# Optimization experiments

Hardware: AMD Instinct MI355X
Metric: run time of the kernel (lower is better)

Reference implementation:

```python
import jax, jax.numpy as jnp
import numpy as np

B, N, E, H, D, FF = 4, 4096, 128, 8, 16, 512
EPS = 1e-6


def rmsnorm(x, w):
    return x * jax.lax.rsqrt(jnp.mean(x * x, axis=-1, keepdims=True) + EPS) * w


def setup_inputs() -> dict:
    key = jax.random.key(0)
    ks = jax.random.split(key, 12)
    s = 1.0 / np.sqrt(E)
    return {
        "x": jax.random.normal(ks[0], (B, N, E), jnp.float32),
        "dis_matrix": jax.random.uniform(ks[1], (B, N, N), jnp.float32),
        "g_in": jnp.ones((E,), jnp.float32),
        "g_post": jnp.ones((E,), jnp.float32),
        "Wq": jax.random.normal(ks[2], (E, E), jnp.float32) * s,
        "Wk": jax.random.normal(ks[3], (E, E), jnp.float32) * s,
        "Wv": jax.random.normal(ks[4], (E, E), jnp.float32) * s,
        "alpha": jnp.float32(1.0),
        "Wo": jax.random.normal(ks[5], (H * D, E), jnp.float32) * s,
        "W1": jax.random.normal(ks[6], (E, FF), jnp.float32) * s,
        "b1": jnp.zeros((FF,), jnp.float32),
        "W2": jax.random.normal(ks[7], (FF, E), jnp.float32) / np.sqrt(FF),
        "b2": jnp.zeros((E,), jnp.float32),
    }


def reference(x, dis_matrix, g_in, g_post, Wq, Wk, Wv, alpha, Wo, W1, b1, W2, b2):
    b, n, e = x.shape
    h = rmsnorm(x, g_in)
    # project and split heads: [B,N,E] -> [B,H,N,D]
    def heads(y):
        return y.reshape(b, n, H, D).transpose(0, 2, 1, 3)
    q = heads(h @ Wq)
    k = heads(h @ Wk)
    v = heads(h @ Wv)
    # distance-decayed kernel weights [B,N,N]
    dis_w = jnp.exp(-alpha * np.log2(n) * dis_matrix)
    kw = jnp.exp(k)  # [B,H,N,D]
    w1 = jnp.einsum('bij,bhik->bhjk', dis_w, kw * v)
    w2 = jnp.einsum('bij,bhik->bhjk', dis_w, kw)
    att = jax.nn.sigmoid(q) * (w1 / w2)  # [B,H,N,D]
    att = att.transpose(0, 2, 1, 3).reshape(b, n, e)
    out1 = x + att @ Wo
    h2 = rmsnorm(out1, g_post)
    ff = jax.nn.relu(h2 @ W1 + b1) @ W2 + b2
    return out1 + ff
```

## Files before the change

kernel.cpp:

```cpp
#include <hip/hip_runtime.h>
#include <stdint.h>


typedef __attribute__((ext_vector_type(8))) short short8;
typedef __attribute__((ext_vector_type(4))) float f32x4;

__device__ __forceinline__ uint16_t f2bf(float f) {
    uint32_t u = __builtin_bit_cast(uint32_t, f);
    u += 0x7fffu + ((u >> 16) & 1u);
    return (uint16_t)(u >> 16);
}
__device__ __forceinline__ float bf2f(uint16_t h) {
    uint32_t u = ((uint32_t)h) << 16;
    return __builtin_bit_cast(float, u);
}
__device__ __forceinline__ f32x4 mfma16(short8 a, short8 b, f32x4 c) {
    return __builtin_amdgcn_mfma_f32_16x16x32_bf16(a, b, c, 0, 0, 0);
}

__global__ __launch_bounds__(256) void k_prep(
    const float* __restrict__ Wq, const float* __restrict__ Wk,
    const float* __restrict__ Wv, const float* __restrict__ Wo,
    const float* __restrict__ W1, const float* __restrict__ W2,
    uint16_t* __restrict__ wqkvT, uint16_t* __restrict__ woT,
    uint16_t* __restrict__ w1T, uint16_t* __restrict__ w2T) {
    int t = blockIdx.x * 256 + threadIdx.x;
    if (t < 49152) {
        int n = t >> 7, k = t & 127;
        const float* W = (n < 128) ? Wq : (n < 256) ? Wk : Wv;
        wqkvT[t] = f2bf(W[k * 128 + (n & 127)]);
    } else if (t < 65536) {
        int i = t - 49152; int e = i >> 7, d = i & 127;
        woT[i] = f2bf(Wo[d * 128 + e]);
    } else if (t < 131072) {
        int i = t - 65536; int f = i >> 7, e = i & 127;
        w1T[i] = f2bf(W1[e * 512 + f]);
    } else if (t < 196608) {
        int i = t - 131072; int e = i >> 9, f = i & 511;
        w2T[i] = f2bf(W2[f * 128 + e]);
    }
}

__global__ __launch_bounds__(256) void k_rms(
    const float* __restrict__ x, const float* __restrict__ g,
    uint16_t* __restrict__ o) {
    int row = blockIdx.x * 4 + (threadIdx.x >> 6);
    int l = threadIdx.x & 63;
    float2 v = *(const float2*)(x + (size_t)row * 128 + l * 2);
    float ss = v.x * v.x + v.y * v.y;
    #pragma unroll
    for (int m = 32; m >= 1; m >>= 1) ss += __shfl_xor(ss, m, 64);
    float rs = rsqrtf(ss * (1.0f / 128.0f) + 1e-6f);
    float2 gv = *(const float2*)(g + l * 2);
    uint32_t lo = (uint32_t)f2bf(v.x * rs * gv.x) |
                  ((uint32_t)f2bf(v.y * rs * gv.y) << 16);
    *(uint32_t*)(o + (size_t)row * 128 + l * 2) = lo;
}

__global__ __launch_bounds__(384) void k_qkv(
    const uint16_t* __restrict__ h, const uint16_t* __restrict__ wqkvT,
    uint16_t* __restrict__ sigq, uint16_t* __restrict__ mcatT) {
    __shared__ __align__(16) char sm[65536];
    uint16_t* Al = (uint16_t*)sm;
    float*    Pl = (float*)sm;
    const int t = threadIdx.x;
    const int i0 = blockIdx.x * 64;
    for (int idx = t; idx < 1024; idx += 384) {
        int row = idx >> 4, c8 = (idx & 15) * 8;
        *(uint4*)&Al[row * 136 + c8] =
            *(const uint4*)(h + (size_t)(i0 + row) * 128 + c8);
    }
    __syncthreads();
    const int w = t >> 6, l = t & 63, ml = l & 15, qd = l >> 4;
    f32x4 acc[4][4];
    f32x4 zv = {0.f, 0.f, 0.f, 0.f};
    #pragma unroll
    for (int a = 0; a < 4; ++a)
        #pragma unroll
        for (int b = 0; b < 4; ++b) acc[a][b] = zv;
    #pragma unroll
    for (int kc = 0; kc < 4; ++kc) {
        short8 af[4], bfr[4];
        #pragma unroll
        for (int fm = 0; fm < 4; ++fm)
            af[fm] = *(const short8*)&Al[(fm * 16 + ml) * 136 + kc * 32 + qd * 8];
        #pragma unroll
        for (int fn = 0; fn < 4; ++fn)
            bfr[fn] = *(const short8*)(wqkvT + (w * 64 + fn * 16 + ml) * 128 + kc * 32 + qd * 8);
        #pragma unroll
        for (int fm = 0; fm < 4; ++fm)
            #pragma unroll
            for (int fn = 0; fn < 4; ++fn)
                acc[fm][fn] = mfma16(af[fm], bfr[fn], acc[fm][fn]);
    }
    __syncthreads();
    const int bb = i0 >> 12, il0 = i0 & 4095;
    if (w < 2) {
        #pragma unroll
        for (int fm = 0; fm < 4; ++fm)
            #pragma unroll
            for (int fn = 0; fn < 4; ++fn)
                #pragma unroll
                for (int r = 0; r < 4; ++r) {
                    int row = fm * 16 + qd * 4 + r;
                    int col = w * 64 + fn * 16 + ml;
                    sigq[(size_t)(i0 + row) * 128 + col] =
                        f2bf(1.f / (1.f + __expf(-acc[fm][fn][r])));
                }
    } else {
        int half = (w < 4) ? 0 : 1;
        int cbase = (w - (half ? 4 : 2)) * 64;
        #pragma unroll
        for (int fm = 0; fm < 4; ++fm)
            #pragma unroll
            for (int fn = 0; fn < 4; ++fn)
                #pragma unroll
                for (int r = 0; r < 4; ++r) {
                    int row = fm * 16 + qd * 4 + r;
                    int col = cbase + fn * 16 + ml;
                    float vv = acc[fm][fn][r];
                    if (!half) vv = __expf(vv);
                    Pl[row * 256 + half * 128 + ((col + row) & 127)] = vv;
                }
    }
    __syncthreads();
    for (int idx = t; idx < 16384; idx += 384) {
        int cc = idx >> 6, il = idx & 63;
        int pc = ((cc & 127) + il) & 127;
        float ekw = Pl[il * 256 + pc];
        float val = (cc < 128) ? ekw * Pl[il * 256 + 128 + pc] : ekw;
        mcatT[((size_t)bb * 256 + cc) * 4096 + il0 + il] = f2bf(val);
    }
}

__global__ __launch_bounds__(512) void k_big(
    const float* __restrict__ dis, const uint16_t* __restrict__ mcatT,
    const float* __restrict__ alpha_p, float* __restrict__ wbuf) {
    __shared__ __align__(16) uint16_t Al[128 * 72];
    __shared__ __align__(16) uint16_t Bl[256 * 72];
    const int t = threadIdx.x;
    const int j0 = blockIdx.x * 128;
    const int b  = blockIdx.y;
    const int sp = blockIdx.z;
    const float c = -12.0f * alpha_p[0];
    const int w = t >> 6, l = t & 63, ml = l & 15, qd = l >> 4;
    const int wm = w >> 2, wn = w & 3;
    const int sj4 = (t & 31) * 4, si0 = (t >> 5) * 4;
    const float* disb = dis + (size_t)b * 4096 * 4096;
    const uint16_t* mb = mcatT + (size_t)b * 256 * 4096;

    f32x4 acc[4][4];
    f32x4 zv = {0.f, 0.f, 0.f, 0.f};
    #pragma unroll
    for (int a = 0; a < 4; ++a)
        #pragma unroll
        for (int q = 0; q < 4; ++q) acc[a][q] = zv;

    for (int ks = 0; ks < 32; ++ks) {
        const int ig = sp * 2048 + ks * 64;
        float dv[4][4];
        #pragma unroll
        for (int r = 0; r < 4; ++r) {
            float4 v = *(const float4*)(disb + (size_t)(ig + si0 + r) * 4096 + j0 + sj4);
            dv[r][0] = v.x; dv[r][1] = v.y; dv[r][2] = v.z; dv[r][3] = v.w;
        }
        __syncthreads();
        #pragma unroll
        for (int jj = 0; jj < 4; ++jj) {
            uint32_t lo = (uint32_t)f2bf(__expf(c * dv[0][jj])) |
                          ((uint32_t)f2bf(__expf(c * dv[1][jj])) << 16);
            uint32_t hi = (uint32_t)f2bf(__expf(c * dv[2][jj])) |
                          ((uint32_t)f2bf(__expf(c * dv[3][jj])) << 16);
            uint2 pk = {lo, hi};
            *(uint2*)&Al[(sj4 + jj) * 72 + si0] = pk;
        }
        #pragma unroll
        for (int ii = 0; ii < 4; ++ii) {
            int idx = t + ii * 512;
            int row = idx >> 3, c8 = (idx & 7) * 8;
            *(uint4*)&Bl[row * 72 + c8] =
                *(const uint4*)(mb + (size_t)row * 4096 + ig + c8);
        }
        __syncthreads();
        #pragma unroll
        for (int kc = 0; kc < 2; ++kc) {
            short8 af[4], bfr[4];
            #pragma unroll
            for (int fm = 0; fm < 4; ++fm)
                af[fm] = *(const short8*)&Al[(wm * 64 + fm * 16 + ml) * 72 + kc * 32 + qd * 8];
            #pragma unroll
            for (int fn = 0; fn < 4; ++fn)
                bfr[fn] = *(const short8*)&Bl[(wn * 64 + fn * 16 + ml) * 72 + kc * 32 + qd * 8];
            #pragma unroll
            for (int fm = 0; fm < 4; ++fm)
                #pragma unroll
                for (int fn = 0; fn < 4; ++fn)
                    acc[fm][fn] = mfma16(af[fm], bfr[fn], acc[fm][fn]);
        }
    }
    float* ob = wbuf + ((size_t)(sp * 4 + b) * 4096 + j0) * 256;
    #pragma unroll
    for (int fm = 0; fm < 4; ++fm)
        #pragma unroll
        for (int fn = 0; fn < 4; ++fn) {
            int col = wn * 64 + fn * 16 + ml;
            #pragma unroll
            for (int r = 0; r < 4; ++r) {
                int rowl = wm * 64 + fm * 16 + qd * 4 + r;
                ob[(size_t)rowl * 256 + col] = acc[fm][fn][r];
            }
        }
}

__global__ __launch_bounds__(256) void k_att(
    const float* __restrict__ wbuf, const uint16_t* __restrict__ sigq,
    const uint16_t* __restrict__ woT, const float* __restrict__ x,
    float* __restrict__ out1) {
    __shared__ __align__(16) uint16_t Al[64 * 136];
    __shared__ __align__(16) uint16_t Bl[128 * 136];
    const int t = threadIdx.x;
    const int i0 = blockIdx.x * 64;
    const int b = i0 >> 12, jl0 = i0 & 4095;
    const float* wb0 = wbuf + ((size_t)b * 4096 + jl0) * 256;
    const float* wb1 = wbuf + ((size_t)(4 + b) * 4096 + jl0) * 256;
    #pragma unroll
    for (int ii = 0; ii < 8; ++ii) {
        int idx = t + ii * 256;
        int row = idx >> 5, c4 = (idx & 31) * 4;
        float4 a0 = *(const float4*)(wb0 + (size_t)row * 256 + c4);
        float4 a1 = *(const float4*)(wb1 + (size_t)row * 256 + c4);
        float4 d0 = *(const float4*)(wb0 + (size_t)row * 256 + 128 + c4);
        float4 d1 = *(const float4*)(wb1 + (size_t)row * 256 + 128 + c4);
        const uint16_t* sq = sigq + (size_t)(i0 + row) * 128 + c4;
        uint32_t lo = (uint32_t)f2bf(bf2f(sq[0]) * (a0.x + a1.x) / (d0.x + d1.x)) |
                      ((uint32_t)f2bf(bf2f(sq[1]) * (a0.y + a1.y) / (d0.y + d1.y)) << 16);
        uint32_t hi = (uint32_t)f2bf(bf2f(sq[2]) * (a0.z + a1.z) / (d0.z + d1.z)) |
                      ((uint32_t)f2bf(bf2f(sq[3]) * (a0.w + a1.w) / (d0.w + d1.w)) << 16);
        uint2 pk = {lo, hi};
        *(uint2*)&Al[row * 136 + c4] = pk;
    }
    #pragma unroll
    for (int ii = 0; ii < 8; ++ii) {
        int idx = t + ii * 256;
        int row = idx >> 4, c8 = (idx & 15) * 8;
        *(uint4*)&Bl[row * 136 + c8] = *(const uint4*)(woT + row * 128 + c8);
    }
    __syncthreads();
    const int w = t >> 6, l = t & 63, ml = l & 15, qd = l >> 4;
    const int wm = w >> 1, wn = w & 1;
    f32x4 acc[2][4];
    f32x4 zv = {0.f, 0.f, 0.f, 0.f};
    #pragma unroll
    for (int a = 0; a < 2; ++a)
        #pragma unroll
        for (int q = 0; q < 4; ++q) acc[a][q] = zv;
    #pragma unroll
    for (int kc = 0; kc < 4; ++kc) {
        short8 af[2], bfr[4];
        #pragma unroll
        for (int fm = 0; fm < 2; ++fm)
            af[fm] = *(const short8*)&Al[(wm * 32 + fm * 16 + ml) * 136 + kc * 32 + qd * 8];
        #pragma unroll
        for (int fn = 0; fn < 4; ++fn)
            bfr[fn] = *(const short8*)&Bl[(wn * 64 + fn * 16 + ml) * 136 + kc * 32 + qd * 8];
        #pragma unroll
        for (int fm = 0; fm < 2; ++fm)
            #pragma unroll
            for (int fn = 0; fn < 4; ++fn)
                acc[fm][fn] = mfma16(af[fm], bfr[fn], acc[fm][fn]);
    }
    #pragma unroll
    for (int fm = 0; fm < 2; ++fm)
        #pragma unroll
        for (int fn = 0; fn < 4; ++fn) {
            int col = wn * 64 + fn * 16 + ml;
            #pragma unroll
            for (int r = 0; r < 4; ++r) {
                int rowl = wm * 32 + fm * 16 + qd * 4 + r;
                size_t o = (size_t)(i0 + rowl) * 128 + col;
                out1[o] = x[o] + acc[fm][fn][r];
            }
        }
}

__global__ __launch_bounds__(256) void k_ff1(
    const uint16_t* __restrict__ h2, const uint16_t* __restrict__ w1T,
    const float* __restrict__ b1, uint16_t* __restrict__ R) {
    __shared__ __align__(16) uint16_t Al[64 * 136];
    __shared__ __align__(16) uint16_t Bl[128 * 136];
    const int t = threadIdx.x;
    const int i0 = blockIdx.x * 64;
    const int nt = blockIdx.y;
    #pragma unroll
    for (int ii = 0; ii < 4; ++ii) {
        int idx = t + ii * 256;
        int row = idx >> 4, c8 = (idx & 15) * 8;
        *(uint4*)&Al[row * 136 + c8] =
            *(const uint4*)(h2 + (size_t)(i0 + row) * 128 + c8);
    }
    #pragma unroll
    for (int ii = 0; ii < 8; ++ii) {
        int idx = t + ii * 256;
        int row = idx >> 4, c8 = (idx & 15) * 8;
        *(uint4*)&Bl[row * 136 + c8] =
            *(const uint4*)(w1T + (size_t)(nt * 128 + row) * 128 + c8);
    }
    __syncthreads();
    const int w = t >> 6, l = t & 63, ml = l & 15, qd = l >> 4;
    const int wm = w >> 1, wn = w & 1;
    f32x4 acc[2][4];
    f32x4 zv = {0.f, 0.f, 0.f, 0.f};
    #pragma unroll
    for (int a = 0; a < 2; ++a)
        #pragma unroll
        for (int q = 0; q < 4; ++q) acc[a][q] = zv;
    #pragma unroll
    for (int kc = 0; kc < 4; ++kc) {
        short8 af[2], bfr[4];
        #pragma unroll
        for (int fm = 0; fm < 2; ++fm)
            af[fm] = *(const short8*)&Al[(wm * 32 + fm * 16 + ml) * 136 + kc * 32 + qd * 8];
        #pragma unroll
        for (int fn = 0; fn < 4; ++fn)
            bfr[fn] = *(const short8*)&Bl[(wn * 64 + fn * 16 + ml) * 136 + kc * 32 + qd * 8];
        #pragma unroll
        for (int fm = 0; fm < 2; ++fm)
            #pragma unroll
            for (int fn = 0; fn < 4; ++fn)
                acc[fm][fn] = mfma16(af[fm], bfr[fn], acc[fm][fn]);
    }
    #pragma unroll
    for (int fm = 0; fm < 2; ++fm)
        #pragma unroll
        for (int fn = 0; fn < 4; ++fn) {
            int col = wn * 64 + fn * 16 + ml;
            int gcol = nt * 128 + col;
            #pragma unroll
            for (int r = 0; r < 4; ++r) {
                int rowl = wm * 32 + fm * 16 + qd * 4 + r;
                R[(size_t)(i0 + rowl) * 512 + gcol] =
                    f2bf(fmaxf(acc[fm][fn][r] + b1[gcol], 0.f));
            }
        }
}

__global__ __launch_bounds__(256) void k_ff2(
    const uint16_t* __restrict__ Rm, const uint16_t* __restrict__ w2T,
    const float* __restrict__ b2, const float* __restrict__ out1,
    float* __restrict__ out) {
    __shared__ __align__(16) uint16_t Al[64 * 136];
    __shared__ __align__(16) uint16_t Bl[128 * 136];
    const int t = threadIdx.x;
    const int i0 = blockIdx.x * 64;
    const int w = t >> 6, l = t & 63, ml = l & 15, qd = l >> 4;
    const int wm = w >> 1, wn = w & 1;
    f32x4 acc[2][4];
    f32x4 zv = {0.f, 0.f, 0.f, 0.f};
    #pragma unroll
    for (int a = 0; a < 2; ++a)
        #pragma unroll
        for (int q = 0; q < 4; ++q) acc[a][q] = zv;
    for (int kb = 0; kb < 4; ++kb) {
        __syncthreads();
        #pragma unroll
        for (int ii = 0; ii < 4; ++ii) {
            int idx = t + ii * 256;
            int row = idx >> 4, c8 = (idx & 15) * 8;
            *(uint4*)&Al[row * 136 + c8] =
                *(const uint4*)(Rm + (size_t)(i0 + row) * 512 + kb * 128 + c8);
        }
        #pragma unroll
        for (int ii = 0; ii < 8; ++ii) {
            int idx = t + ii * 256;
            int row = idx >> 4, c8 = (idx & 15) * 8;
            *(uint4*)&Bl[row * 136 + c8] =
                *(const uint4*)(w2T + (size_t)row * 512 + kb * 128 + c8);
        }
        __syncthreads();
        #pragma unroll
        for (int kc = 0; kc < 4; ++kc) {
            short8 af[2], bfr[4];
            #pragma unroll
            for (int fm = 0; fm < 2; ++fm)
                af[fm] = *(const short8*)&Al[(wm * 32 + fm * 16 + ml) * 136 + kc * 32 + qd * 8];
            #pragma unroll
            for (int fn = 0; fn < 4; ++fn)
                bfr[fn] = *(const short8*)&Bl[(wn * 64 + fn * 16 + ml) * 136 + kc * 32 + qd * 8];
            #pragma unroll
            for (int fm = 0; fm < 2; ++fm)
                #pragma unroll
                for (int fn = 0; fn < 4; ++fn)
                    acc[fm][fn] = mfma16(af[fm], bfr[fn], acc[fm][fn]);
        }
    }
    #pragma unroll
    for (int fm = 0; fm < 2; ++fm)
        #pragma unroll
        for (int fn = 0; fn < 4; ++fn) {
            int col = wn * 64 + fn * 16 + ml;
            #pragma unroll
            for (int r = 0; r < 4; ++r) {
                int rowl = wm * 32 + fm * 16 + qd * 4 + r;
                size_t o = (size_t)(i0 + rowl) * 128 + col;
                out[o] = out1[o] + b2[col] + acc[fm][fn][r];
            }
        }
}

extern "C" void kernel_launch(void* const* d_in, const int* in_sizes, int n_in,
                              void* d_out, int out_size, void* d_ws, size_t ws_size,
                              hipStream_t stream) {
    (void)in_sizes; (void)n_in; (void)out_size; (void)ws_size;
    const float* x      = (const float*)d_in[0];
    const float* dis    = (const float*)d_in[1];
    const float* g_in   = (const float*)d_in[2];
    const float* g_post = (const float*)d_in[3];
    const float* Wq     = (const float*)d_in[4];
    const float* Wk     = (const float*)d_in[5];
    const float* Wv     = (const float*)d_in[6];
    const float* alpha  = (const float*)d_in[7];
    const float* Wo     = (const float*)d_in[8];
    const float* W1     = (const float*)d_in[9];
    const float* b1     = (const float*)d_in[10];
    const float* W2     = (const float*)d_in[11];
    const float* b2     = (const float*)d_in[12];
    float* out = (float*)d_out;

    char* ws = (char*)d_ws;
    size_t off = 0;
    auto take = [&](size_t bytes) -> char* {
        char* p = ws + off;
        off += (bytes + 255) & ~(size_t)255;
        return p;
    };
    uint16_t* h     = (uint16_t*)take(16384ull * 128 * 2);
    uint16_t* wqkvT = (uint16_t*)take(384ull * 128 * 2);
    uint16_t* woT   = (uint16_t*)take(128ull * 128 * 2);
    uint16_t* w1T   = (uint16_t*)take(512ull * 128 * 2);
    uint16_t* w2T   = (uint16_t*)take(128ull * 512 * 2);
    uint16_t* sigq  = (uint16_t*)take(16384ull * 128 * 2);
    uint16_t* mcatT = (uint16_t*)take(4ull * 256 * 4096 * 2);
    float*    wbuf  = (float*)take(2ull * 4 * 4096 * 256 * 4);
    float*    out1  = (float*)take(16384ull * 128 * 4);
    uint16_t* h2    = (uint16_t*)take(16384ull * 128 * 2);
    uint16_t* R     = (uint16_t*)take(16384ull * 512 * 2);

    k_prep<<<768, 256, 0, stream>>>(Wq, Wk, Wv, Wo, W1, W2, wqkvT, woT, w1T, w2T);
    k_rms<<<4096, 256, 0, stream>>>(x, g_in, h);
    k_qkv<<<256, 384, 0, stream>>>(h, wqkvT, sigq, mcatT);
    k_big<<<dim3(32, 4, 2), 512, 0, stream>>>(dis, mcatT, alpha, wbuf);
    k_att<<<256, 256, 0, stream>>>(wbuf, sigq, woT, x, out1);
    k_rms<<<4096, 256, 0, stream>>>(out1, g_post, h2);
    k_ff1<<<dim3(256, 4), 256, 0, stream>>>(h2, w1T, b1, R);
    k_ff2<<<256, 256, 0, stream>>>(R, w2T, b2, out1, out);
}
```

Measured before the change: 467.1 us.

## Fuse distance-kernel GEMM with attention epilogue, Wo, RMSNorm; fuse FF layers

Replaces the split-K big GEMM plus separate attention, RMSNorm and two FF kernels with one kernel that computes the full K range per 32-column tile. That kernel register-prefetches the next dis/mcat tile, then applies the sigmoid-q ratio, the Wo projection, the residual and the post-RMSNorm in-block. A second kernel fuses FF1, ReLU and FF2, keeping the hidden activations in shared memory, so the wbuf and R intermediates and three launches go away. The risk is that the smaller 32-wide tiles give less MFMA reuse per block and only a quarter of the threads do the exp conversion, and the grid drops from 256 large blocks to 512 smaller ones with no split-K.

After: 699.3 us. 49.7% more time.

```diff
diff --git a/kernel.cpp b/kernel.cpp
--- a/kernel.cpp
+++ b/kernel.cpp
@@ -133,276 +133,255 @@
     }
 }
 
-__global__ __launch_bounds__(512) void k_big(
+__global__ __launch_bounds__(512, 4) void k_mega(
     const float* __restrict__ dis, const uint16_t* __restrict__ mcatT,
-    const float* __restrict__ alpha_p, float* __restrict__ wbuf) {
-    __shared__ __align__(16) uint16_t Al[128 * 72];
-    __shared__ __align__(16) uint16_t Bl[256 * 72];
+    const float* __restrict__ alpha_p, const uint16_t* __restrict__ sigq,
+    const uint16_t* __restrict__ woT, const float* __restrict__ x,
+    const float* __restrict__ g_post,
+    float* __restrict__ out1, uint16_t* __restrict__ h2) {
+    __shared__ __align__(16) char sm[42496];
+    uint16_t* Al = (uint16_t*)sm;
+    uint16_t* Bl = (uint16_t*)(sm + 4608);
+    float*    P  = (float*)sm;
+    uint16_t* Att= (uint16_t*)(sm + 33792);
+    __shared__ float rowsum[32];
+
     const int t = threadIdx.x;
-    const int j0 = blockIdx.x * 128;
+    const int j0 = blockIdx.x * 32;
     const int b  = blockIdx.y;
-    const int sp = blockIdx.z;
     const float c = -12.0f * alpha_p[0];
     const int w = t >> 6, l = t & 63, ml = l & 15, qd = l >> 4;
-    const int wm = w >> 2, wn = w & 3;
-    const int sj4 = (t & 31) * 4, si0 = (t >> 5) * 4;
-    const float* disb = dis + (size_t)b * 4096 * 4096;
+    const bool aload = (t < 128);
+    const int sj4 = (t & 7) * 4, si0 = ((t >> 3) & 15) * 4;
+    const float* disb = dis + (size_t)b * 4096 * 4096 + j0;
     const uint16_t* mb = mcatT + (size_t)b * 256 * 4096;
 
-    f32x4 acc[4][4];
+    f32x4 acc[2][2];
     f32x4 zv = {0.f, 0.f, 0.f, 0.f};
-    #pragma unroll
-    for (int a = 0; a < 4; ++a)
-        #pragma unroll
-        for (int q = 0; q < 4; ++q) acc[a][q] = zv;
-
-    for (int ks = 0; ks < 32; ++ks) {
-        const int ig = sp * 2048 + ks * 64;
-        float dv[4][4];
+    acc[0][0] = zv; acc[0][1] = zv; acc[1][0] = zv; acc[1][1] = zv;
+
+    float dv[4][4];
+    uint4 mc[4];
+    if (aload) {
         #pragma unroll
         for (int r = 0; r < 4; ++r) {
-            float4 v = *(const float4*)(disb + (size_t)(ig + si0 + r) * 4096 + j0 + sj4);
+            float4 v = *(const float4*)(disb + (size_t)(si0 + r) * 4096 + sj4);
             dv[r][0] = v.x; dv[r][1] = v.y; dv[r][2] = v.z; dv[r][3] = v.w;
         }
+    }
+    #pragma unroll
+    for (int ii = 0; ii < 4; ++ii) {
+        int idx = t + ii * 512;
+        int row = idx >> 3, c8 = (idx & 7) * 8;
+        mc[ii] = *(const uint4*)(mb + (size_t)row * 4096 + c8);
+    }
+
+    for (int ks = 0; ks < 64; ++ks) {
         __syncthreads();
-        #pragma unroll
-        for (int jj = 0; jj < 4; ++jj) {
-            uint32_t lo = (uint32_t)f2bf(__expf(c * dv[0][jj])) |
-                          ((uint32_t)f2bf(__expf(c * dv[1][jj])) << 16);
-            uint32_t hi = (uint32_t)f2bf(__expf(c * dv[2][jj])) |
-                          ((uint32_t)f2bf(__expf(c * dv[3][jj])) << 16);
-            uint2 pk = {lo, hi};
-            *(uint2*)&Al[(sj4 + jj) * 72 + si0] = pk;
+        if (aload) {
+            #pragma unroll
+            for (int jj = 0; jj < 4; ++jj) {
+                uint32_t lo = (uint32_t)f2bf(__expf(c * dv[0][jj])) |
+                              ((uint32_t)f2bf(__expf(c * dv[1][jj])) << 16);
+                uint32_t hi = (uint32_t)f2bf(__expf(c * dv[2][jj])) |
+                              ((uint32_t)f2bf(__expf(c * dv[3][jj])) << 16);
+                uint2 pk = {lo, hi};
+                *(uint2*)&Al[(sj4 + jj) * 72 + si0] = pk;
+            }
         }
         #pragma unroll
         for (int ii = 0; ii < 4; ++ii) {
             int idx = t + ii * 512;
             int row = idx >> 3, c8 = (idx & 7) * 8;
-            *(uint4*)&Bl[row * 72 + c8] =
-                *(const uint4*)(mb + (size_t)row * 4096 + ig + c8);
+            *(uint4*)&Bl[row * 72 + c8] = mc[ii];
         }
         __syncthreads();
+        if (ks < 63) {
+            const int ig = (ks + 1) * 64;
+            if (aload) {
+                #pragma unroll
+                for (int r = 0; r < 4; ++r) {
+                    float4 v = *(const float4*)(disb + (size_t)(ig + si0 + r) * 4096 + sj4);
+                    dv[r][0] = v.x; dv[r][1] = v.y; dv[r][2] = v.z; dv[r][3] = v.w;
+                }
+            }
+            #pragma unroll
+            for (int ii = 0; ii < 4; ++ii) {
+                int idx = t + ii * 512;
+                int row = idx >> 3, c8 = (idx & 7) * 8;
+                mc[ii] = *(const uint4*)(mb + (size_t)row * 4096 + ig + c8);
+            }
+        }
         #pragma unroll
         for (int kc = 0; kc < 2; ++kc) {
-            short8 af[4], bfr[4];
-            #pragma unroll
-            for (int fm = 0; fm < 4; ++fm)
-                af[fm] = *(const short8*)&Al[(wm * 64 + fm * 16 + ml) * 72 + kc * 32 + qd * 8];
-            #pragma unroll
-            for (int fn = 0; fn < 4; ++fn)
-                bfr[fn] = *(const short8*)&Bl[(wn * 64 + fn * 16 + ml) * 72 + kc * 32 + qd * 8];
-            #pragma unroll
-            for (int fm = 0; fm < 4; ++fm)
-                #pragma unroll
-                for (int fn = 0; fn < 4; ++fn)
-                    acc[fm][fn] = mfma16(af[fm], bfr[fn], acc[fm][fn]);
-        }
-    }
-    float* ob = wbuf + ((size_t)(sp * 4 + b) * 4096 + j0) * 256;
-    #pragma unroll
-    for (int fm = 0; fm < 4; ++fm)
-        #pragma unroll
-        for (int fn = 0; fn < 4; ++fn) {
-            int col = wn * 64 + fn * 16 + ml;
-            #pragma unroll
-            for (int r = 0; r < 4; ++r) {
-                int rowl = wm * 64 + fm * 16 + qd * 4 + r;
-                ob[(size_t)rowl * 256 + col] = acc[fm][fn][r];
-            }
-        }
-}
-
-__global__ __launch_bounds__(256) void k_att(
-    const float* __restrict__ wbuf, const uint16_t* __restrict__ sigq,
-    const uint16_t* __restrict__ woT, const float* __restrict__ x,
-    float* __restrict__ out1) {
+            short8 af0 = *(const short8*)&Al[(ml) * 72 + kc * 32 + qd * 8];
+            short8 af1 = *(const short8*)&Al[(16 + ml) * 72 + kc * 32 + qd * 8];
+            short8 bf0 = *(const short8*)&Bl[(w * 32 + ml) * 72 + kc * 32 + qd * 8];
+            short8 bf1 = *(const short8*)&Bl[(w * 32 + 16 + ml) * 72 + kc * 32 + qd * 8];
+            acc[0][0] = mfma16(af0, bf0, acc[0][0]);
+            acc[0][1] = mfma16(af0, bf1, acc[0][1]);
+            acc[1][0] = mfma16(af1, bf0, acc[1][0]);
+            acc[1][1] = mfma16(af1, bf1, acc[1][1]);
+        }
+    }
+
+    __syncthreads();
+    {
+        const int colb = w * 32;
+        #pragma unroll
+        for (int fm = 0; fm < 2; ++fm)
+            #pragma unroll
+            for (int fn = 0; fn < 2; ++fn) {
+                int col = colb + fn * 16 + ml;
+                #pragma unroll
+                for (int r = 0; r < 4; ++r)
+                    P[(fm * 16 + qd * 4 + r) * 264 + col] = acc[fm][fn][r];
+            }
+    }
+    if (t < 32) rowsum[t] = 0.f;
+    __syncthreads();
+    {
+        const uint16_t* sq = sigq + (size_t)(b * 4096 + j0) * 128;
+        #pragma unroll
+        for (int it = 0; it < 2; ++it) {
+            int q = t + it * 512;
+            int j = q >> 5, c4 = (q & 31) * 4;
+            float4 w1v = *(const float4*)&P[j * 264 + c4];
+            float4 w2v = *(const float4*)&P[j * 264 + 128 + c4];
+            const uint16_t* sp = sq + j * 128 + c4;
+            uint32_t lo = (uint32_t)f2bf(bf2f(sp[0]) * w1v.x / w2v.x) |
+                          ((uint32_t)f2bf(bf2f(sp[1]) * w1v.y / w2v.y) << 16);
+            uint32_t hi = (uint32_t)f2bf(bf2f(sp[2]) * w1v.z / w2v.z) |
+                          ((uint32_t)f2bf(bf2f(sp[3]) * w1v.w / w2v.w) << 16);
+            uint2 pk = {lo, hi};
+            *(uint2*)&Att[j * 136 + c4] = pk;
+        }
+    }
+    __syncthreads();
+    f32x4 acc2[2];
+    acc2[0] = zv; acc2[1] = zv;
+    #pragma unroll
+    for (int kc = 0; kc < 4; ++kc) {
+        short8 af0 = *(const short8*)&Att[(ml) * 136 + kc * 32 + qd * 8];
+        short8 af1 = *(const short8*)&Att[(16 + ml) * 136 + kc * 32 + qd * 8];
+        short8 bf  = *(const short8*)(woT + (w * 16 + ml) * 128 + kc * 32 + qd * 8);
+        acc2[0] = mfma16(af0, bf, acc2[0]);
+        acc2[1] = mfma16(af1, bf, acc2[1]);
+    }
+    const int col = w * 16 + ml;
+    const float gp = g_post[col];
+    float ov[2][4];
+    #pragma unroll
+    for (int fm = 0; fm < 2; ++fm)
+        #pragma unroll
+        for (int r = 0; r < 4; ++r) {
+            int rowl = fm * 16 + qd * 4 + r;
+            size_t o = (size_t)(b * 4096 + j0 + rowl) * 128 + col;
+            float v = x[o] + acc2[fm][r];
+            ov[fm][r] = v;
+            out1[o] = v;
+            float ss = v * v;
+            ss += __shfl_xor(ss, 1, 64);
+            ss += __shfl_xor(ss, 2, 64);
+            ss += __shfl_xor(ss, 4, 64);
+            ss += __shfl_xor(ss, 8, 64);
+            if (ml == 0) atomicAdd(&rowsum[rowl], ss);
+        }
+    __syncthreads();
+    #pragma unroll
+    for (int fm = 0; fm < 2; ++fm)
+        #pragma unroll
+        for (int r = 0; r < 4; ++r) {
+            int rowl = fm * 16 + qd * 4 + r;
+            float rs = rsqrtf(rowsum[rowl] * (1.f / 128.f) + 1e-6f);
+            h2[(size_t)(b * 4096 + j0 + rowl) * 128 + col] = f2bf(ov[fm][r] * rs * gp);
+        }
+}
+
+__global__ __launch_bounds__(512) void k_ff(
+    const uint16_t* __restrict__ h2, const uint16_t* __restrict__ w1T,
+    const float* __restrict__ b1, const uint16_t* __restrict__ w2T,
+    const float* __restrict__ b2, const float* __restrict__ out1,
+    float* __restrict__ out) {
     __shared__ __align__(16) uint16_t Al[64 * 136];
-    __shared__ __align__(16) uint16_t Bl[128 * 136];
+    __shared__ __align__(16) uint16_t Rl[64 * 264];
     const int t = threadIdx.x;
     const int i0 = blockIdx.x * 64;
-    const int b = i0 >> 12, jl0 = i0 & 4095;
-    const float* wb0 = wbuf + ((size_t)b * 4096 + jl0) * 256;
-    const float* wb1 = wbuf + ((size_t)(4 + b) * 4096 + jl0) * 256;
-    #pragma unroll
-    for (int ii = 0; ii < 8; ++ii) {
-        int idx = t + ii * 256;
-        int row = idx >> 5, c4 = (idx & 31) * 4;
-        float4 a0 = *(const float4*)(wb0 + (size_t)row * 256 + c4);
-        float4 a1 = *(const float4*)(wb1 + (size_t)row * 256 + c4);
-        float4 d0 = *(const float4*)(wb0 + (size_t)row * 256 + 128 + c4);
-        float4 d1 = *(const float4*)(wb1 + (size_t)row * 256 + 128 + c4);
-        const uint16_t* sq = sigq + (size_t)(i0 + row) * 128 + c4;
-        uint32_t lo = (uint32_t)f2bf(bf2f(sq[0]) * (a0.x + a1.x) / (d0.x + d1.x)) |
-                      ((uint32_t)f2bf(bf2f(sq[1]) * (a0.y + a1.y) / (d0.y + d1.y)) << 16);
-        uint32_t hi = (uint32_t)f2bf(bf2f(sq[2]) * (a0.z + a1.z) / (d0.z + d1.z)) |
-                      ((uint32_t)f2bf(bf2f(sq[3]) * (a0.w + a1.w) / (d0.w + d1.w)) << 16);
-        uint2 pk = {lo, hi};
-        *(uint2*)&Al[row * 136 + c4] = pk;
-    }
-    #pragma unroll
-    for (int ii = 0; ii < 8; ++ii) {
-        int idx = t + ii * 256;
-        int row = idx >> 4, c8 = (idx & 15) * 8;
-        *(uint4*)&Bl[row * 136 + c8] = *(const uint4*)(woT + row * 128 + c8);
-    }
-    __syncthreads();
     const int w = t >> 6, l = t & 63, ml = l & 15, qd = l >> 4;
-    const int wm = w >> 1, wn = w & 1;
-    f32x4 acc[2][4];
-    f32x4 zv = {0.f, 0.f, 0.f, 0.f};
-    #pragma unroll
-    for (int a = 0; a < 2; ++a)
-        #pragma unroll
-        for (int q = 0; q < 4; ++q) acc[a][q] = zv;
-    #pragma unroll
-    for (int kc = 0; kc < 4; ++kc) {
-        short8 af[2], bfr[4];
-        #pragma unroll
-        for (int fm = 0; fm < 2; ++fm)
-            af[fm] = *(const short8*)&Al[(wm * 32 + fm * 16 + ml) * 136 + kc * 32 + qd * 8];
-        #pragma unroll
-        for (int fn = 0; fn < 4; ++fn)
-            bfr[fn] = *(const short8*)&Bl[(wn * 64 + fn * 16 + ml) * 136 + kc * 32 + qd * 8];
-        #pragma unroll
-        for (int fm = 0; fm < 2; ++fm)
-            #pragma unroll
-            for (int fn = 0; fn < 4; ++fn)
-                acc[fm][fn] = mfma16(af[fm], bfr[fn], acc[fm][fn]);
-    }
-    #pragma unroll
-    for (int fm = 0; fm < 2; ++fm)
-        #pragma unroll
-        for (int fn = 0; fn < 4; ++fn) {
-            int col = wn * 64 + fn * 16 + ml;
-            #pragma unroll
-            for (int r = 0; r < 4; ++r) {
-                int rowl = wm * 32 + fm * 16 + qd * 4 + r;
-                size_t o = (size_t)(i0 + rowl) * 128 + col;
-                out1[o] = x[o] + acc[fm][fn][r];
-            }
-        }
-}
-
-__global__ __launch_bounds__(256) void k_ff1(
-    const uint16_t* __restrict__ h2, const uint16_t* __restrict__ w1T,
-    const float* __restrict__ b1, uint16_t* __restrict__ R) {
-    __shared__ __align__(16) uint16_t Al[64 * 136];
-    __shared__ __align__(16) uint16_t Bl[128 * 136];
-    const int t = threadIdx.x;
-    const int i0 = blockIdx.x * 64;
-    const int nt = blockIdx.y;
-    #pragma unroll
-    for (int ii = 0; ii < 4; ++ii) {
-        int idx = t + ii * 256;
+    #pragma unroll
+    for (int ii = 0; ii < 2; ++ii) {
+        int idx = t + ii * 512;
         int row = idx >> 4, c8 = (idx & 15) * 8;
         *(uint4*)&Al[row * 136 + c8] =
             *(const uint4*)(h2 + (size_t)(i0 + row) * 128 + c8);
     }
-    #pragma unroll
-    for (int ii = 0; ii < 8; ++ii) {
-        int idx = t + ii * 256;
-        int row = idx >> 4, c8 = (idx & 15) * 8;
-        *(uint4*)&Bl[row * 136 + c8] =
-            *(const uint4*)(w1T + (size_t)(nt * 128 + row) * 128 + c8);
-    }
-    __syncthreads();
-    const int w = t >> 6, l = t & 63, ml = l & 15, qd = l >> 4;
-    const int wm = w >> 1, wn = w & 1;
-    f32x4 acc[2][4];
+    __syncthreads();
+    const int wm = w >> 2, wn = w & 3;
     f32x4 zv = {0.f, 0.f, 0.f, 0.f};
-    #pragma unroll
-    for (int a = 0; a < 2; ++a)
-        #pragma unroll
-        for (int q = 0; q < 4; ++q) acc[a][q] = zv;
-    #pragma unroll
-    for (int kc = 0; kc < 4; ++kc) {
-        short8 af[2], bfr[4];
-        #pragma unroll
-        for (int fm = 0; fm < 2; ++fm)
-            af[fm] = *(const short8*)&Al[(wm * 32 + fm * 16 + ml) * 136 + kc * 32 + qd * 8];
-        #pragma unroll
-        for (int fn = 0; fn < 4; ++fn)
-            bfr[fn] = *(const short8*)&Bl[(wn * 64 + fn * 16 + ml) * 136 + kc * 32 + qd * 8];
-        #pragma unroll
-        for (int fm = 0; fm < 2; ++fm)
-            #pragma unroll
-            for (int fn = 0; fn < 4; ++fn)
-                acc[fm][fn] = mfma16(af[fm], bfr[fn], acc[fm][fn]);
+    f32x4 a2[2][2];
+    a2[0][0] = zv; a2[0][1] = zv; a2[1][0] = zv; a2[1][1] = zv;
+    for (int hf = 0; hf < 2; ++hf) {
+        if (hf) __syncthreads();
+        f32x4 a1[4][2];
+        #pragma unroll
+        for (int fm = 0; fm < 4; ++fm) { a1[fm][0] = zv; a1[fm][1] = zv; }
+        #pragma unroll
+        for (int kc = 0; kc < 4; ++kc) {
+            short8 af[4], bfr[2];
+            #pragma unroll
+            for (int fm = 0; fm < 4; ++fm)
+                af[fm] = *(const short8*)&Al[(fm * 16 + ml) * 136 + kc * 32 + qd * 8];
+            #pragma unroll
+            for (int fn = 0; fn < 2; ++fn)
+                bfr[fn] = *(const short8*)(w1T +
+                    (size_t)(hf * 256 + w * 32 + fn * 16 + ml) * 128 + kc * 32 + qd * 8);
+            #pragma unroll
+            for (int fm = 0; fm < 4; ++fm)
+                #pragma unroll
+                for (int fn = 0; fn < 2; ++fn)
+                    a1[fm][fn] = mfma16(af[fm], bfr[fn], a1[fm][fn]);
+        }
+        #pragma unroll
+        for (int fm = 0; fm < 4; ++fm)
+            #pragma unroll
+            for (int fn = 0; fn < 2; ++fn) {
+                int fcol = w * 32 + fn * 16 + ml;
+                float bias = b1[hf * 256 + fcol];
+                #pragma unroll
+                for (int r = 0; r < 4; ++r) {
+                    int row = fm * 16 + qd * 4 + r;
+                    Rl[row * 264 + fcol] = f2bf(fmaxf(a1[fm][fn][r] + bias, 0.f));
+                }
+            }
+        __syncthreads();
+        #pragma unroll
+        for (int kc = 0; kc < 8; ++kc) {
+            short8 af[2], bfr[2];
+            #pragma unroll
+            for (int fm = 0; fm < 2; ++fm)
+                af[fm] = *(const short8*)&Rl[(wm * 32 + fm * 16 + ml) * 264 + kc * 32 + qd * 8];
+            #pragma unroll
+            for (int fn = 0; fn < 2; ++fn)
+                bfr[fn] = *(const short8*)(w2T +
+                    (size_t)(wn * 32 + fn * 16 + ml) * 512 + hf * 256 + kc * 32 + qd * 8);
+            #pragma unroll
+            for (int fm = 0; fm < 2; ++fm)
+                #pragma unroll
+                for (int fn = 0; fn < 2; ++fn)
+                    a2[fm][fn] = mfma16(af[fm], bfr[fn], a2[fm][fn]);
+        }
     }
     #pragma unroll
     for (int fm = 0; fm < 2; ++fm)
         #pragma unroll
-        for (int fn = 0; fn < 4; ++fn) {
-            int col = wn * 64 + fn * 16 + ml;
-            int gcol = nt * 128 + col;
+        for (int fn = 0; fn < 2; ++fn) {
+            int colo = wn * 32 + fn * 16 + ml;
+            float bias = b2[colo];
             #pragma unroll
             for (int r = 0; r < 4; ++r) {
                 int rowl = wm * 32 + fm * 16 + qd * 4 + r;
-                R[(size_t)(i0 + rowl) * 512 + gcol] =
-                    f2bf(fmaxf(acc[fm][fn][r] + b1[gcol], 0.f));
-            }
-        }
-}
-
-__global__ __launch_bounds__(256) void k_ff2(
-    const uint16_t* __restrict__ Rm, const uint16_t* __restrict__ w2T,
-    const float* __restrict__ b2, const float* __restrict__ out1,
-    float* __restrict__ out) {
-    __shared__ __align__(16) uint16_t Al[64 * 136];
-    __shared__ __align__(16) uint16_t Bl[128 * 136];
-    const int t = threadIdx.x;
-    const int i0 = blockIdx.x * 64;
-    const int w = t >> 6, l = t & 63, ml = l & 15, qd = l >> 4;
-    const int wm = w >> 1, wn = w & 1;
-    f32x4 acc[2][4];
-    f32x4 zv = {0.f, 0.f, 0.f, 0.f};
-    #pragma unroll
-    for (int a = 0; a < 2; ++a)
-        #pragma unroll
-        for (int q = 0; q < 4; ++q) acc[a][q] = zv;
-    for (int kb = 0; kb < 4; ++kb) {
-        __syncthreads();
-        #pragma unroll
-        for (int ii = 0; ii < 4; ++ii) {
-            int idx = t + ii * 256;
-            int row = idx >> 4, c8 = (idx & 15) * 8;
-            *(uint4*)&Al[row * 136 + c8] =
-                *(const uint4*)(Rm + (size_t)(i0 + row) * 512 + kb * 128 + c8);
-        }
-        #pragma unroll
-        for (int ii = 0; ii < 8; ++ii) {
-            int idx = t + ii * 256;
-            int row = idx >> 4, c8 = (idx & 15) * 8;
-            *(uint4*)&Bl[row * 136 + c8] =
-                *(const uint4*)(w2T + (size_t)row * 512 + kb * 128 + c8);
-        }
-        __syncthreads();
-        #pragma unroll
-        for (int kc = 0; kc < 4; ++kc) {
-            short8 af[2], bfr[4];
-            #pragma unroll
-            for (int fm = 0; fm < 2; ++fm)
-                af[fm] = *(const short8*)&Al[(wm * 32 + fm * 16 + ml) * 136 + kc * 32 + qd * 8];
-            #pragma unroll
-            for (int fn = 0; fn < 4; ++fn)
-                bfr[fn] = *(const short8*)&Bl[(wn * 64 + fn * 16 + ml) * 136 + kc * 32 + qd * 8];
-            #pragma unroll
-            for (int fm = 0; fm < 2; ++fm)
-                #pragma unroll
-                for (int fn = 0; fn < 4; ++fn)
-                    acc[fm][fn] = mfma16(af[fm], bfr[fn], acc[fm][fn]);
-        }
-    }
-    #pragma unroll
-    for (int fm = 0; fm < 2; ++fm)
-        #pragma unroll
-        for (int fn = 0; fn < 4; ++fn) {
-            int col = wn * 64 + fn * 16 + ml;
-            #pragma unroll
-            for (int r = 0; r < 4; ++r) {
-                int rowl = wm * 32 + fm * 16 + qd * 4 + r;
-                size_t o = (size_t)(i0 + rowl) * 128 + col;
-                out[o] = out1[o] + b2[col] + acc[fm][fn][r];
+                size_t o = (size_t)(i0 + rowl) * 128 + colo;
+                out[o] = out1[o] + bias + a2[fm][fn][r];
             }
         }
 }
@@ -440,17 +419,12 @@
     uint16_t* w2T   = (uint16_t*)take(128ull * 512 * 2);
     uint16_t* sigq  = (uint16_t*)take(16384ull * 128 * 2);
     uint16_t* mcatT = (uint16_t*)take(4ull * 256 * 4096 * 2);
-    float*    wbuf  = (float*)take(2ull * 4 * 4096 * 256 * 4);
     float*    out1  = (float*)take(16384ull * 128 * 4);
     uint16_t* h2    = (uint16_t*)take(16384ull * 128 * 2);
-    uint16_t* R     = (uint16_t*)take(16384ull * 512 * 2);
 
     k_prep<<<768, 256, 0, stream>>>(Wq, Wk, Wv, Wo, W1, W2, wqkvT, woT, w1T, w2T);
     k_rms<<<4096, 256, 0, stream>>>(x, g_in, h);
     k_qkv<<<256, 384, 0, stream>>>(h, wqkvT, sigq, mcatT);
-    k_big<<<dim3(32, 4, 2), 512, 0, stream>>>(dis, mcatT, alpha, wbuf);
-    k_att<<<256, 256, 0, stream>>>(wbuf, sigq, woT, x, out1);
-    k_rms<<<4096, 256, 0, stream>>>(out1, g_post, h2);
-    k_ff1<<<dim3(256, 4), 256, 0, stream>>>(h2, w1T, b1, R);
-    k_ff2<<<256, 256, 0, stream>>>(R, w2T, b2, out1, out);
-}
+    k_mega<<<dim3(128, 4), 512, 0, stream>>>(dis, mcatT, alpha, sigq, woT, x, g_post, out1, h2);
+    k_ff<<<256, 512, 0, stream>>>(h2, w1T, b1, w2T, b2, out1, out);
+}
```
